# Kernel tuning notes

Hardware: AMD Instinct MI355X
Metric: run time of the kernel (lower is better)

The kernel has to match this reference:

```python
import jax, jax.numpy as jnp
import numpy as np

B_, L_, D_, N_ = 2, 2048, 512, 64

def setup_inputs() -> dict:
    key = jax.random.key(0)
    ks = jax.random.split(key, 6)
    s = 1.0 / np.sqrt(D_)
    return {
        "x": jax.random.normal(ks[0], (B_, L_, D_), dtype=jnp.float32),
        "W1": jax.random.normal(ks[1], (D_, D_), dtype=jnp.float32) * s,
        "b1": jnp.zeros((D_,), dtype=jnp.float32),
        "W2": jax.random.normal(ks[2], (D_, N_), dtype=jnp.float32) * s,
        "b2": jnp.zeros((N_,), dtype=jnp.float32),
        "W3": jax.random.normal(ks[3], (D_, N_), dtype=jnp.float32) * s,
        "b3": jnp.zeros((N_,), dtype=jnp.float32),
        "A": jax.random.normal(ks[4], (D_, N_), dtype=jnp.float32) * (1.0 / np.sqrt(N_)),
    }

def reference(x, W1, b1, W2, b2, W3, b3, A):
    # Projections (faithful to fc2/fc3/fc1 in the torch module)
    B = x @ W2 + b2                                  # (b, l, n)
    C = x @ W3 + b3                                  # (b, l, n)
    delta = jax.nn.softplus(x @ W1 + b1)             # (b, l, d)
    # Discretization
    dB = jnp.einsum('bld,bln->bldn', delta, B)       # (b, l, d, n)
    dA = jnp.exp(jnp.einsum('bld,dn->bldn', delta, A))  # (b, l, d, n)
    # h is initialized to zeros in the original forward, so the dA*h term
    # contributes exactly zero; kept for faithfulness to the source math.
    h = dA * 0.0 + x[..., None] * dB                 # (b, l, d, n)
    y = jnp.einsum('bln,bldn->bld', C, h)            # (b, l, d)
    return y
```

## Files before the change

### kernel.cpp

```cpp
#include <hip/hip_runtime.h>
#include <math.h>

#define DDIM 512

typedef _Float16 f16;
typedef _Float16 f16x4 __attribute__((ext_vector_type(4)));
typedef _Float16 f16x8 __attribute__((ext_vector_type(8)));
typedef float f32x4 __attribute__((ext_vector_type(4)));

__device__ __forceinline__ float softplusf(float v) {
    return (v > 20.0f) ? v : log1pf(__expf(v));
}

__global__ __launch_bounds__(256) void prep_w(
    const float* __restrict__ W1, const float* __restrict__ W2,
    const float* __restrict__ W3, f16* __restrict__ w1t, f16* __restrict__ w23)
{
    __shared__ __align__(16) f16 lt[32][520];
    const int tid  = threadIdx.x;
    const int wb   = blockIdx.x;
    const int wv   = tid >> 6;
    const int lane = tid & 63;
    const int q    = lane >> 4;
    const int l15  = lane & 15;

    const float* src; int srcRS, col0; f16* dst;
    if (wb < 16)      { src = W1; srcRS = DDIM; col0 = wb * 32;
                        dst = w1t + (size_t)wb * 2 * 16 * 512; }
    else if (wb < 18) { src = W2; srcRS = 64;  col0 = (wb - 16) * 32;
                        dst = w23 + (size_t)(wb - 16) * 2 * 16 * 512; }
    else              { src = W3; srcRS = 64;  col0 = (wb - 18) * 32;
                        dst = w23 + (size_t)(4 + (wb - 18) * 2) * 16 * 512; }
#pragma unroll
    for (int i = 0; i < 16; ++i) {
        int f  = tid + 256 * i;
        int k  = f >> 3;
        int c4 = (f & 7) * 4;
        float4 v = *(const float4*)(src + (size_t)k * srcRS + col0 + c4);
        lt[c4 + 0][k] = (f16)v.x; lt[c4 + 1][k] = (f16)v.y;
        lt[c4 + 2][k] = (f16)v.z; lt[c4 + 3][k] = (f16)v.w;
    }
    __syncthreads();
#pragma unroll
    for (int j = 0; j < 8; ++j) {
        int s   = wv * 8 + j;
        int ntL = s >> 4;
        int kt  = s & 15;
        f16x8 vv = *(const f16x8*)&lt[ntL * 16 + l15][kt * 32 + q * 8];
        *(f16x8*)(dst + (size_t)(ntL * 16 + kt) * 512 + lane * 8) = vv;
    }
}

__global__ __launch_bounds__(256) void s_kernel(
    const float* __restrict__ x, const f16* __restrict__ w23,
    const float* __restrict__ b2, const float* __restrict__ b3,
    f16* __restrict__ xh, float* __restrict__ s_out)
{
    __shared__ __align__(16) f16 xs[16][520];
    __shared__ float sred[64];

    const int tid  = threadIdx.x;
    const int wv   = tid >> 6;
    const int lane = tid & 63;
    const int q    = lane >> 4;
    const int l15  = lane & 15;
    const int mtG  = blockIdx.x;
    const int tb   = mtG * 16;

    {
        const int row = tid >> 4, cg = tid & 15;
        const float* xr = x + (size_t)(tb + row) * DDIM;
#pragma unroll
        for (int i = 0; i < 8; ++i) {
            int col = cg * 4 + i * 64;
            float4 v = *(const float4*)(xr + col);
            f16x4 h = {(f16)v.x, (f16)v.y, (f16)v.z, (f16)v.w};
            *(f16x4*)&xs[row][col] = h;
        }
    }
    __syncthreads();

#pragma unroll
    for (int j = 0; j < 4; ++j) {
        int kt = wv * 4 + j;
        f16x8 vv = *(const f16x8*)&xs[l15][kt * 32 + q * 8];
        *(f16x8*)(xh + (size_t)(mtG * 16 + kt) * 512 + lane * 8) = vv;
    }

    f32x4 acc0 = (f32x4){0.f, 0.f, 0.f, 0.f};
    f32x4 acc1 = (f32x4){0.f, 0.f, 0.f, 0.f};
    const f16* wB = w23 + (size_t)(wv    ) * 16 * 512 + lane * 8;
    const f16* wC = w23 + (size_t)(wv + 4) * 16 * 512 + lane * 8;
#pragma unroll
    for (int kt = 0; kt < 16; ++kt) {
        f16x8 a  = *(const f16x8*)&xs[l15][kt * 32 + q * 8];
        f16x8 bB = *(const f16x8*)(wB + (size_t)kt * 512);
        f16x8 bC = *(const f16x8*)(wC + (size_t)kt * 512);
        acc0 = __builtin_amdgcn_mfma_f32_16x16x32_f16(a, bB, acc0, 0, 0, 0);
        acc1 = __builtin_amdgcn_mfma_f32_16x16x32_f16(a, bC, acc1, 0, 0, 0);
    }

    float b2v = b2[wv * 16 + l15];
    float b3v = b3[wv * 16 + l15];
#pragma unroll
    for (int r = 0; r < 4; ++r) {
        float p = (acc0[r] + b2v) * (acc1[r] + b3v);
        p += __shfl_xor(p, 1); p += __shfl_xor(p, 2);
        p += __shfl_xor(p, 4); p += __shfl_xor(p, 8);
        if (l15 == 0) sred[wv * 16 + q * 4 + r] = p;
    }
    __syncthreads();
    if (tid < 16)
        s_out[tb + tid] = sred[tid] + sred[16 + tid] + sred[32 + tid] + sred[48 + tid];
}

__global__ __launch_bounds__(512) void y_kernel(
    const f16* __restrict__ xh, const f16* __restrict__ w1t,
    const float* __restrict__ x, const float* __restrict__ b1,
    const float* __restrict__ s_in, float* __restrict__ y)
{
    const int tid  = threadIdx.x;
    const int wv   = tid >> 6;
    const int lane = tid & 63;
    const int q    = lane >> 4;
    const int l15  = lane & 15;
    const int mt   = wv & 3;
    const int nh   = wv >> 2;
    const int cB   = blockIdx.x;
    const int rB   = blockIdx.y;

    const f16* aP  = xh  + (size_t)((rB * 4 + mt) * 16) * 512 + lane * 8;
    const f16* bP0 = w1t + (size_t)((cB * 4 + nh * 2 + 0) * 16) * 512 + lane * 8;
    const f16* bP1 = w1t + (size_t)((cB * 4 + nh * 2 + 1) * 16) * 512 + lane * 8;

    f32x4 acc0 = (f32x4){0.f, 0.f, 0.f, 0.f};
    f32x4 acc1 = (f32x4){0.f, 0.f, 0.f, 0.f};
#pragma unroll
    for (int kt = 0; kt < 16; ++kt) {
        f16x8 a  = *(const f16x8*)(aP  + (size_t)kt * 512);
        f16x8 b0 = *(const f16x8*)(bP0 + (size_t)kt * 512);
        f16x8 b1v = *(const f16x8*)(bP1 + (size_t)kt * 512);
        acc0 = __builtin_amdgcn_mfma_f32_16x16x32_f16(a, b0,  acc0, 0, 0, 0);
        acc1 = __builtin_amdgcn_mfma_f32_16x16x32_f16(a, b1v, acc1, 0, 0, 0);
    }

    const int d0 = cB * 64 + (nh * 2 + 0) * 16 + l15;
    const int d1 = cB * 64 + (nh * 2 + 1) * 16 + l15;
    const float bb0 = b1[d0], bb1 = b1[d1];
#pragma unroll
    for (int r = 0; r < 4; ++r) {
        int token = rB * 64 + mt * 16 + q * 4 + r;
        float st = s_in[token];
        const float* xr = x + (size_t)token * DDIM;
        float*       yr = y + (size_t)token * DDIM;
        yr[d0] = xr[d0] * softplusf(acc0[r] + bb0) * st;
        yr[d1] = xr[d1] * softplusf(acc1[r] + bb1) * st;
    }
}

extern "C" void kernel_launch(void* const* d_in, const int* in_sizes, int n_in,
                              void* d_out, int out_size, void* d_ws, size_t ws_size,
                              hipStream_t stream)
{
    (void)n_in; (void)out_size; (void)ws_size;
    const float* x  = (const float*)d_in[0];
    const float* W1 = (const float*)d_in[1];
    const float* b1 = (const float*)d_in[2];
    const float* W2 = (const float*)d_in[3];
    const float* b2 = (const float*)d_in[4];
    const float* W3 = (const float*)d_in[5];
    const float* b3 = (const float*)d_in[6];
    float* y = (float*)d_out;

    char* ws  = (char*)d_ws;
    f16* xh   = (f16*)(ws);
    f16* w1t  = (f16*)(ws + (4 << 20));
    f16* w23  = (f16*)(ws + (4 << 20) + (512 << 10));
    float* sv = (float*)(ws + (5 << 20));

    const int M = in_sizes[0] / DDIM;

    prep_w<<<20, 256, 0, stream>>>(W1, W2, W3, w1t, w23);
    s_kernel<<<M / 16, 256, 0, stream>>>(x, w23, b2, b3, xh, sv);
    y_kernel<<<dim3(8, M / 64), 512, 0, stream>>>(xh, w1t, x, b1, sv, y);
}
```

Measured before the change: 95.92 us.

## Fuse S-reduction and Y GEMM kernels into one per-16-token block kernel

Merges s_kernel and y_kernel into a single kernel where each 512-thread block loads 16 tokens of x into LDS once, in both fp32 and fp16. The block computes the B/C projections and the s dot product locally, then the full 512-column W1 GEMM, and writes y through coalesced float4 stores staged in LDS. This removes the xh and s workspace round trips, one launch, and the strided scalar y writes. In exchange, each block re-reads all of W1 (512 KB fp16) from L2, and the grid shrinks to 256 blocks that each use heavy LDS, which lowers occupancy.

```diff
diff --git a/kernel.cpp b/kernel.cpp
--- a/kernel.cpp
+++ b/kernel.cpp
@@ -51,110 +51,104 @@
     }
 }
 
-__global__ __launch_bounds__(256) void s_kernel(
-    const float* __restrict__ x, const f16* __restrict__ w23,
+__global__ __launch_bounds__(512) void fused_sy(
+    const float* __restrict__ x, const f16* __restrict__ w1t,
+    const f16* __restrict__ w23, const float* __restrict__ b1,
     const float* __restrict__ b2, const float* __restrict__ b3,
-    f16* __restrict__ xh, float* __restrict__ s_out)
+    float* __restrict__ y)
 {
-    __shared__ __align__(16) f16 xs[16][520];
-    __shared__ float sred[64];
+    __shared__ __align__(16) float xf[16][516];
+    __shared__ __align__(16) f16  xs[16][520];
+    __shared__ float sp[8][16][17];
+    __shared__ float s_lds[16];
 
     const int tid  = threadIdx.x;
     const int wv   = tid >> 6;
     const int lane = tid & 63;
     const int q    = lane >> 4;
     const int l15  = lane & 15;
-    const int mtG  = blockIdx.x;
-    const int tb   = mtG * 16;
+    const int tb   = blockIdx.x * 16;
+
+#pragma unroll
+    for (int it = 0; it < 4; ++it) {
+        int f   = tid + 512 * it;
+        int row = f >> 7;
+        int c4  = (f & 127) * 4;
+        float4 v = *(const float4*)(x + (size_t)(tb + row) * DDIM + c4);
+        *(float4*)&xf[row][c4] = v;
+        f16x4 h = {(f16)v.x, (f16)v.y, (f16)v.z, (f16)v.w};
+        *(f16x4*)&xs[row][c4] = h;
+    }
+    __syncthreads();
 
     {
-        const int row = tid >> 4, cg = tid & 15;
-        const float* xr = x + (size_t)(tb + row) * DDIM;
+        const f16* wS = w23 + (size_t)wv * 16 * 512 + lane * 8;
+        f32x4 aclo = (f32x4){0.f, 0.f, 0.f, 0.f};
+        f32x4 achi = (f32x4){0.f, 0.f, 0.f, 0.f};
 #pragma unroll
-        for (int i = 0; i < 8; ++i) {
-            int col = cg * 4 + i * 64;
-            float4 v = *(const float4*)(xr + col);
-            f16x4 h = {(f16)v.x, (f16)v.y, (f16)v.z, (f16)v.w};
-            *(f16x4*)&xs[row][col] = h;
+        for (int kt = 0; kt < 8; ++kt) {
+            f16x8 a0 = *(const f16x8*)&xs[l15][kt * 32 + q * 8];
+            f16x8 a1 = *(const f16x8*)&xs[l15][(kt + 8) * 32 + q * 8];
+            f16x8 w0 = *(const f16x8*)(wS + (size_t)kt * 512);
+            f16x8 w1 = *(const f16x8*)(wS + (size_t)(kt + 8) * 512);
+            aclo = __builtin_amdgcn_mfma_f32_16x16x32_f16(a0, w0, aclo, 0, 0, 0);
+            achi = __builtin_amdgcn_mfma_f32_16x16x32_f16(a1, w1, achi, 0, 0, 0);
+        }
+        float bias = (wv < 4) ? b2[wv * 16 + l15] : b3[(wv - 4) * 16 + l15];
+#pragma unroll
+        for (int r = 0; r < 4; ++r)
+            sp[wv][q * 4 + r][l15] = aclo[r] + achi[r] + bias;
+    }
+    __syncthreads();
+
+    if (tid < 256) {
+        int t = tid >> 4, n16 = tid & 15;
+        float v = 0.f;
+#pragma unroll
+        for (int g = 0; g < 4; ++g)
+            v += sp[g][t][n16] * sp[4 + g][t][n16];
+        v += __shfl_xor(v, 1); v += __shfl_xor(v, 2);
+        v += __shfl_xor(v, 4); v += __shfl_xor(v, 8);
+        if (n16 == 0) s_lds[t] = v;
+    }
+
+    f32x4 acc[4];
+#pragma unroll
+    for (int i = 0; i < 4; ++i) acc[i] = (f32x4){0.f, 0.f, 0.f, 0.f};
+    const f16* bP = w1t + (size_t)(wv * 4) * 16 * 512 + lane * 8;
+#pragma unroll
+    for (int kt = 0; kt < 16; ++kt) {
+        f16x8 a  = *(const f16x8*)&xs[l15][kt * 32 + q * 8];
+        f16x8 f0 = *(const f16x8*)(bP + (size_t)(0 * 16 + kt) * 512);
+        f16x8 f1 = *(const f16x8*)(bP + (size_t)(1 * 16 + kt) * 512);
+        f16x8 f2 = *(const f16x8*)(bP + (size_t)(2 * 16 + kt) * 512);
+        f16x8 f3 = *(const f16x8*)(bP + (size_t)(3 * 16 + kt) * 512);
+        acc[0] = __builtin_amdgcn_mfma_f32_16x16x32_f16(a, f0, acc[0], 0, 0, 0);
+        acc[1] = __builtin_amdgcn_mfma_f32_16x16x32_f16(a, f1, acc[1], 0, 0, 0);
+        acc[2] = __builtin_amdgcn_mfma_f32_16x16x32_f16(a, f2, acc[2], 0, 0, 0);
+        acc[3] = __builtin_amdgcn_mfma_f32_16x16x32_f16(a, f3, acc[3], 0, 0, 0);
+    }
+    __syncthreads();
+
+#pragma unroll
+    for (int i = 0; i < 4; ++i) {
+        int d = (wv * 4 + i) * 16 + l15;
+        float bb = b1[d];
+#pragma unroll
+        for (int r = 0; r < 4; ++r) {
+            int t = q * 4 + r;
+            xf[t][d] = xf[t][d] * softplusf(acc[i][r] + bb) * s_lds[t];
         }
     }
     __syncthreads();
 
 #pragma unroll
-    for (int j = 0; j < 4; ++j) {
-        int kt = wv * 4 + j;
-        f16x8 vv = *(const f16x8*)&xs[l15][kt * 32 + q * 8];
-        *(f16x8*)(xh + (size_t)(mtG * 16 + kt) * 512 + lane * 8) = vv;
-    }
-
-    f32x4 acc0 = (f32x4){0.f, 0.f, 0.f, 0.f};
-    f32x4 acc1 = (f32x4){0.f, 0.f, 0.f, 0.f};
-    const f16* wB = w23 + (size_t)(wv    ) * 16 * 512 + lane * 8;
-    const f16* wC = w23 + (size_t)(wv + 4) * 16 * 512 + lane * 8;
-#pragma unroll
-    for (int kt = 0; kt < 16; ++kt) {
-        f16x8 a  = *(const f16x8*)&xs[l15][kt * 32 + q * 8];
-        f16x8 bB = *(const f16x8*)(wB + (size_t)kt * 512);
-        f16x8 bC = *(const f16x8*)(wC + (size_t)kt * 512);
-        acc0 = __builtin_amdgcn_mfma_f32_16x16x32_f16(a, bB, acc0, 0, 0, 0);
-        acc1 = __builtin_amdgcn_mfma_f32_16x16x32_f16(a, bC, acc1, 0, 0, 0);
-    }
-
-    float b2v = b2[wv * 16 + l15];
-    float b3v = b3[wv * 16 + l15];
-#pragma unroll
-    for (int r = 0; r < 4; ++r) {
-        float p = (acc0[r] + b2v) * (acc1[r] + b3v);
-        p += __shfl_xor(p, 1); p += __shfl_xor(p, 2);
-        p += __shfl_xor(p, 4); p += __shfl_xor(p, 8);
-        if (l15 == 0) sred[wv * 16 + q * 4 + r] = p;
-    }
-    __syncthreads();
-    if (tid < 16)
-        s_out[tb + tid] = sred[tid] + sred[16 + tid] + sred[32 + tid] + sred[48 + tid];
-}
-
-__global__ __launch_bounds__(512) void y_kernel(
-    const f16* __restrict__ xh, const f16* __restrict__ w1t,
-    const float* __restrict__ x, const float* __restrict__ b1,
-    const float* __restrict__ s_in, float* __restrict__ y)
-{
-    const int tid  = threadIdx.x;
-    const int wv   = tid >> 6;
-    const int lane = tid & 63;
-    const int q    = lane >> 4;
-    const int l15  = lane & 15;
-    const int mt   = wv & 3;
-    const int nh   = wv >> 2;
-    const int cB   = blockIdx.x;
-    const int rB   = blockIdx.y;
-
-    const f16* aP  = xh  + (size_t)((rB * 4 + mt) * 16) * 512 + lane * 8;
-    const f16* bP0 = w1t + (size_t)((cB * 4 + nh * 2 + 0) * 16) * 512 + lane * 8;
-    const f16* bP1 = w1t + (size_t)((cB * 4 + nh * 2 + 1) * 16) * 512 + lane * 8;
-
-    f32x4 acc0 = (f32x4){0.f, 0.f, 0.f, 0.f};
-    f32x4 acc1 = (f32x4){0.f, 0.f, 0.f, 0.f};
-#pragma unroll
-    for (int kt = 0; kt < 16; ++kt) {
-        f16x8 a  = *(const f16x8*)(aP  + (size_t)kt * 512);
-        f16x8 b0 = *(const f16x8*)(bP0 + (size_t)kt * 512);
-        f16x8 b1v = *(const f16x8*)(bP1 + (size_t)kt * 512);
-        acc0 = __builtin_amdgcn_mfma_f32_16x16x32_f16(a, b0,  acc0, 0, 0, 0);
-        acc1 = __builtin_amdgcn_mfma_f32_16x16x32_f16(a, b1v, acc1, 0, 0, 0);
-    }
-
-    const int d0 = cB * 64 + (nh * 2 + 0) * 16 + l15;
-    const int d1 = cB * 64 + (nh * 2 + 1) * 16 + l15;
-    const float bb0 = b1[d0], bb1 = b1[d1];
-#pragma unroll
-    for (int r = 0; r < 4; ++r) {
-        int token = rB * 64 + mt * 16 + q * 4 + r;
-        float st = s_in[token];
-        const float* xr = x + (size_t)token * DDIM;
-        float*       yr = y + (size_t)token * DDIM;
-        yr[d0] = xr[d0] * softplusf(acc0[r] + bb0) * st;
-        yr[d1] = xr[d1] * softplusf(acc1[r] + bb1) * st;
+    for (int it = 0; it < 4; ++it) {
+        int f   = tid + 512 * it;
+        int row = f >> 7;
+        int c4  = (f & 127) * 4;
+        *(float4*)(y + (size_t)(tb + row) * DDIM + c4) =
+            *(const float4*)&xf[row][c4];
     }
 }
 
@@ -172,15 +166,12 @@
     const float* b3 = (const float*)d_in[6];
     float* y = (float*)d_out;
 
-    char* ws  = (char*)d_ws;
-    f16* xh   = (f16*)(ws);
-    f16* w1t  = (f16*)(ws + (4 << 20));
-    f16* w23  = (f16*)(ws + (4 << 20) + (512 << 10));
-    float* sv = (float*)(ws + (5 << 20));
+    char* ws = (char*)d_ws;
+    f16* w1t = (f16*)ws;
+    f16* w23 = (f16*)(ws + (512 << 10));
 
     const int M = in_sizes[0] / DDIM;
 
     prep_w<<<20, 256, 0, stream>>>(W1, W2, W3, w1t, w23);
-    s_kernel<<<M / 16, 256, 0, stream>>>(x, w23, b2, b3, xh, sv);
-    y_kernel<<<dim3(8, M / 64), 512, 0, stream>>>(xh, w1t, x, b1, sv, y);
+    fused_sy<<<M / 16, 512, 0, stream>>>(x, w1t, w23, b1, b2, b3, y);
 }
```

Result: faster. 93.72 us (-2.3%).
